# Kernel optimization log

Measured on AMD Instinct MI355X. Metric: run time of the kernel, lower is better.

## Reference

```python
import jax, jax.numpy as jnp
import numpy as np

B, S, H, DH = 2, 4096, 8, 64
D = H * DH  # 512

def setup_inputs() -> dict:
    key = jax.random.key(0)
    ks = jax.random.split(key, 9)
    sc = 1.0 / np.sqrt(D)
    return {
        "hidden_states": jax.random.normal(ks[0], (B, S, D), jnp.float32),
        "Wq": jax.random.normal(ks[1], (D, D), jnp.float32) * sc,
        "bq": jax.random.normal(ks[2], (D,), jnp.float32) * 0.02,
        "Wk": jax.random.normal(ks[3], (D, D), jnp.float32) * sc,
        "bk": jax.random.normal(ks[4], (D,), jnp.float32) * 0.02,
        "Wv": jax.random.normal(ks[5], (D, D), jnp.float32) * sc,
        "bv": jax.random.normal(ks[6], (D,), jnp.float32) * 0.02,
        "Wo": jax.random.normal(ks[7], (D, D), jnp.float32) * sc,
        "bo": jax.random.normal(ks[8], (D,), jnp.float32) * 0.02,
    }

def _split_heads(t):
    # (B, S, H*DH) -> (B, H, S, DH)
    b = t.shape[0]
    return t.reshape(b, S, H, DH).transpose(0, 2, 1, 3)

def reference(hidden_states, Wq, bq, Wk, bk, Wv, bv, Wo, bo):
    q = _split_heads(hidden_states @ Wq + bq)
    k = _split_heads(hidden_states @ Wk + bk)
    v = _split_heads(hidden_states @ Wv + bv)
    scale = 1.0 / jnp.sqrt(jnp.asarray(DH, q.dtype))
    energy = jnp.einsum('bhqd,bhkd->bhqk', q, k) * scale
    weights = jax.nn.softmax(energy, axis=-1)  # full O(S^2) matrix, as in source
    attended = jnp.einsum('bhqv,bhvd->bhqd', weights, v)
    merged = attended.transpose(0, 2, 1, 3).reshape(hidden_states.shape[0], S, D)
    return merged @ Wo + bo
```

## Files before the change

### kernel.cpp

```cpp
#include <hip/hip_runtime.h>
#include <cstdint>

typedef __bf16 bf16;
typedef __bf16 bf16x4 __attribute__((ext_vector_type(4)));
typedef __bf16 bf16x8 __attribute__((ext_vector_type(8)));
typedef float floatx4 __attribute__((ext_vector_type(4)));

#define MFMA32(a, b, c) __builtin_amdgcn_mfma_f32_16x16x32_bf16((a), (b), (c), 0, 0, 0)

__device__ inline bf16x8 cvt8(const float* p) {
    float4 u = *(const float4*)p;
    float4 v = *(const float4*)(p + 4);
    bf16x8 r;
    r[0] = (bf16)u.x; r[1] = (bf16)u.y; r[2] = (bf16)u.z; r[3] = (bf16)u.w;
    r[4] = (bf16)v.x; r[5] = (bf16)v.y; r[6] = (bf16)v.z; r[7] = (bf16)v.w;
    return r;
}

__global__ __launch_bounds__(256) void k_transpose(
    const float* __restrict__ w0, const float* __restrict__ w1,
    const float* __restrict__ w2, const float* __restrict__ w3,
    bf16* __restrict__ o0, bf16* __restrict__ o1,
    bf16* __restrict__ o2, bf16* __restrict__ o3)
{
    __shared__ float t[32][33];
    const float* in;
    bf16* out;
    switch (blockIdx.z) {
        case 0: in = w0; out = o0; break;
        case 1: in = w1; out = o1; break;
        case 2: in = w2; out = o2; break;
        default: in = w3; out = o3; break;
    }
    const int tx = threadIdx.x & 31;
    const int ty = threadIdx.x >> 5;
    const int r0 = blockIdx.y * 32;
    const int c0 = blockIdx.x * 32;
    #pragma unroll
    for (int i = 0; i < 32; i += 8)
        t[ty + i][tx] = in[(size_t)(r0 + ty + i) * 512 + c0 + tx];
    __syncthreads();
    #pragma unroll
    for (int i = 0; i < 32; i += 8)
        out[(size_t)(c0 + ty + i) * 512 + r0 + tx] = (bf16)t[tx][ty + i];
}

__global__ __launch_bounds__(256) void k_cvtx(
    const float* __restrict__ X, bf16* __restrict__ Xb)
{
    const size_t idx = ((size_t)blockIdx.x * 256 + threadIdx.x) * 8;
    *(bf16x8*)(Xb + idx) = cvt8(X + idx);
}

__global__ __launch_bounds__(256) void k_qkv(
    const bf16* __restrict__ Xb, const bf16* __restrict__ Wcat,
    const float* __restrict__ bq, const float* __restrict__ bk, const float* __restrict__ bv,
    bf16* __restrict__ Qs, bf16* __restrict__ Ks, bf16* __restrict__ Vt)
{
    __shared__ __align__(16) unsigned char smem[36864];
    uint4* Al = (uint4*)smem;
    uint4* Bl = (uint4*)(smem + 16384);

    const int tid  = threadIdx.x;
    const int w    = tid >> 6;
    const int lane = tid & 63;
    const int col  = lane & 15;
    const int quad = lane >> 4;
    const int m0 = blockIdx.x * 128;
    const int n0 = blockIdx.y * 128;

    const bf16* gA0 = Xb   + (size_t)(m0 + (tid >> 2)) * 512 + (tid & 3) * 8;
    const bf16* gA1 = gA0 + 64 * 512;
    const bf16* gB0 = Wcat + (size_t)(n0 + (tid >> 2)) * 512 + (tid & 3) * 8;
    const bf16* gB1 = gB0 + 64 * 512;

    const floatx4 zf = {0.f, 0.f, 0.f, 0.f};
    floatx4 acc[4][4];
    #pragma unroll
    for (int a = 0; a < 4; ++a)
        #pragma unroll
        for (int b = 0; b < 4; ++b) acc[a][b] = zf;

    Al[tid]       = *(const uint4*)gA0;
    Al[tid + 256] = *(const uint4*)gA1;
    Bl[tid]       = *(const uint4*)gB0;
    Bl[tid + 256] = *(const uint4*)gB1;
    __syncthreads();

    const int mb = (w & 1) * 64;
    const int nb = (w >> 1) * 64;

    int buf = 0;
    for (int kk = 0; kk < 16; ++kk) {
        const int kn = ((kk + 1) & 15) * 32;
        const uint4 pa0 = *(const uint4*)(gA0 + kn);
        const uint4 pa1 = *(const uint4*)(gA1 + kn);
        const uint4 pb0 = *(const uint4*)(gB0 + kn);
        const uint4 pb1 = *(const uint4*)(gB1 + kn);

        const uint4* A4 = Al + buf * 512;
        const uint4* B4 = Bl + buf * 512;
        bf16x8 af[4], bfr[4];
        #pragma unroll
        for (int t = 0; t < 4; ++t) {
            union { uint4 u; bf16x8 v; } ca, cb;
            ca.u = A4[(mb + 16 * t + col) * 4 + quad];
            cb.u = B4[(nb + 16 * t + col) * 4 + quad];
            af[t] = ca.v;
            bfr[t] = cb.v;
        }
        #pragma unroll
        for (int tm = 0; tm < 4; ++tm)
            #pragma unroll
            for (int tn = 0; tn < 4; ++tn)
                acc[tm][tn] = MFMA32(af[tm], bfr[tn], acc[tm][tn]);

        const int nbuf = buf ^ 1;
        Al[nbuf * 512 + tid]       = pa0;
        Al[nbuf * 512 + tid + 256] = pa1;
        Bl[nbuf * 512 + tid]       = pb0;
        Bl[nbuf * 512 + tid + 256] = pb1;
        __syncthreads();
        buf = nbuf;
    }

    bf16* ep = (bf16*)smem + (size_t)w * 64 * 72;

    const int which = blockIdx.y >> 2;
    const int nbase = (blockIdx.y & 3) * 128 + nb;
    const int h  = nbase >> 6;
    const int mw = m0 + mb;
    const int b  = mw >> 12;
    const int s0 = mw & 4095;
    const float qsc = 0.125f * 1.44269504088896f;

    if (which == 2) {
        #pragma unroll
        for (int tn = 0; tn < 4; ++tn) {
            const int d = 16 * tn + col;
            const float bb = bv[nbase + d];
            #pragma unroll
            for (int tm = 0; tm < 4; ++tm) {
                union { bf16 e[4]; uint2 u; } pk;
                #pragma unroll
                for (int r = 0; r < 4; ++r) pk.e[r] = (bf16)(acc[tm][tn][r] + bb);
                *(uint2*)(ep + d * 72 + 16 * tm + 4 * quad) = pk.u;
            }
        }
    } else {
        const float* bias = (which == 0) ? bq : bk;
        const float sc = (which == 0) ? qsc : 1.0f;
        #pragma unroll
        for (int tn = 0; tn < 4; ++tn) {
            const int d = 16 * tn + col;
            const float bb = bias[nbase + d];
            #pragma unroll
            for (int tm = 0; tm < 4; ++tm)
                #pragma unroll
                for (int r = 0; r < 4; ++r)
                    ep[(16 * tm + 4 * quad + r) * 72 + d] = (bf16)((acc[tm][tn][r] + bb) * sc);
        }
    }

    asm volatile("" ::: "memory");

    const int rl = lane >> 3;
    const int ch = lane & 7;
    bf16* gbase;
    size_t rowstride;
    if (which == 2) {
        gbase = Vt + (((size_t)b * 8 + h) * 64) * 4096 + s0;
        rowstride = 4096;
    } else {
        bf16* P = (which == 0) ? Qs : Ks;
        gbase = P + (((size_t)b * 8 + h) * 4096 + s0) * 64;
        rowstride = 64;
    }
    #pragma unroll
    for (int it = 0; it < 8; ++it) {
        const int row = it * 8 + rl;
        const uint4 v = *(const uint4*)(ep + row * 72 + ch * 8);
        *(uint4*)(gbase + (size_t)row * rowstride + ch * 8) = v;
    }
}

__global__ __launch_bounds__(512, 4) void k_attn(
    const bf16* __restrict__ Qs, const bf16* __restrict__ Ks, const bf16* __restrict__ Vt,
    bf16* __restrict__ att)
{
    __shared__ __align__(16) unsigned char smem[33280];
    uint4* Klds = (uint4*)smem;
    uint4* Vlds = (uint4*)(smem + 16384);
    float* Of   = (float*)smem;
    float* Ls   = (float*)(smem + 32768);

    const int tid  = threadIdx.x;
    const int w    = tid >> 6;
    const int hf   = w >> 2;
    const int wq   = w & 3;
    const int lane = tid & 63;
    const int col  = lane & 15;
    const int quad = lane >> 4;
    const int i    = blockIdx.x;
    const int bh   = ((i & 7) << 1) | ((i >> 3) & 1);
    const int q0   = (i >> 4) * 128 + wq * 32;

    const bf16* Qb = Qs + (size_t)bh * 262144;
    const bf16* Kb = Ks + (size_t)bh * 262144 + (size_t)hf * 2048 * 64;
    const bf16* Vb = Vt + (size_t)bh * 262144 + (size_t)hf * 2048;

    const int t8  = tid & 255;
    const int rK  = t8 >> 3;
    const int lcK = (t8 & 7) ^ (rK & 7);
    const bf16* gK = Kb + (size_t)rK * 64 + lcK * 8;
    const int pV  = t8 >> 3;
    const int ccV = (t8 & 7) ^ (pV & 7);
    const int dV  = 2 * pV + (ccV >> 2);
    const int cV  = ccV & 3;
    const bf16* gV = Vb + (size_t)dV * 4096 + cV * 8;

    uint4* Kl2 = Klds + hf * 512;
    uint4* Vl2 = Vlds + hf * 512;

    bf16x8 aq[2][2];
    #pragma unroll
    for (int s = 0; s < 2; ++s)
        #pragma unroll
        for (int c = 0; c < 2; ++c)
            aq[s][c] = *(const bf16x8*)(Qb + (size_t)(q0 + 16 * s + col) * 64 + 32 * c + quad * 8);

    const floatx4 zf = {0.f, 0.f, 0.f, 0.f};
    floatx4 o[2][4];
    float lsum[2] = {0.f, 0.f};
    #pragma unroll
    for (int s = 0; s < 2; ++s)
        #pragma unroll
        for (int dt = 0; dt < 4; ++dt) o[s][dt] = zf;

    const int c1 = col & 1, ch2 = col >> 1, qh = quad >> 1, ql = quad & 1;

    Kl2[t8] = *(const uint4*)gK;
    Vl2[t8] = *(const uint4*)gV;
    __syncthreads();

    int buf = 0;
    for (int kt = 0; kt < 2048; kt += 32) {
        const int kn = (kt + 32) & 2047;
        const uint4 kreg = *(const uint4*)(gK + (size_t)kn * 64);
        const uint4 vreg = *(const uint4*)(gV + kn);

        const uint4* Kl = Kl2 + buf * 256;
        const uint2* Vl = (const uint2*)(Vl2 + buf * 256);

        bf16x8 kf[2][2];
        #pragma unroll
        for (int t = 0; t < 2; ++t)
            #pragma unroll
            for (int c = 0; c < 2; ++c) {
                union { uint4 u; bf16x8 v; } cv;
                cv.u = Kl[(16 * t + col) * 8 + ((quad + 4 * c) ^ (col & 7))];
                kf[t][c] = cv.v;
            }
        bf16x8 vfrag8[4];
        #pragma unroll
        for (int dt = 0; dt < 4; ++dt) {
            union { uint2 u[2]; bf16x8 v; } cv;
            #pragma unroll
            for (int t = 0; t < 2; ++t) {
                const int slot = (dt * 8 + ch2) * 8 + ((c1 * 4 + 2 * t + qh) ^ ch2);
                cv.u[t] = Vl[slot * 2 + ql];
            }
            vfrag8[dt] = cv.v;
        }

        #pragma unroll
        for (int s = 0; s < 2; ++s) {
            union { bf16 e[8]; bf16x8 v; } pw;
            #pragma unroll
            for (int t = 0; t < 2; ++t) {
                floatx4 sc = MFMA32(kf[t][1], aq[s][1], MFMA32(kf[t][0], aq[s][0], zf));
                const float p0 = __builtin_amdgcn_exp2f(sc[0]);
                const float p1 = __builtin_amdgcn_exp2f(sc[1]);
                const float p2 = __builtin_amdgcn_exp2f(sc[2]);
                const float p3 = __builtin_amdgcn_exp2f(sc[3]);
                lsum[s] += (p0 + p1) + (p2 + p3);
                pw.e[4 * t + 0] = (bf16)p0; pw.e[4 * t + 1] = (bf16)p1;
                pw.e[4 * t + 2] = (bf16)p2; pw.e[4 * t + 3] = (bf16)p3;
            }
            #pragma unroll
            for (int dt = 0; dt < 4; ++dt)
                o[s][dt] = MFMA32(vfrag8[dt], pw.v, o[s][dt]);
        }

        Kl2[(buf ^ 1) * 256 + t8] = kreg;
        Vl2[(buf ^ 1) * 256 + t8] = vreg;
        __syncthreads();
        buf ^= 1;
    }

    float lv[2];
    #pragma unroll
    for (int s = 0; s < 2; ++s) {
        float v = lsum[s];
        v += __shfl_xor(v, 16, 64);
        v += __shfl_xor(v, 32, 64);
        lv[s] = v;
    }

    float* op = Of + ((size_t)(wq * 64 + lane)) * 32;
    if (hf == 1) {
        #pragma unroll
        for (int s = 0; s < 2; ++s)
            #pragma unroll
            for (int dt = 0; dt < 4; ++dt) {
                const int f = s * 4 + dt;
                *(floatx4*)(op + ((f + lane) & 7) * 4) = o[s][dt];
            }
        if (quad == 0) {
            Ls[(wq * 2 + 0) * 16 + col] = lv[0];
            Ls[(wq * 2 + 1) * 16 + col] = lv[1];
        }
    }
    __syncthreads();
    if (hf == 0) {
        float inv[2];
        #pragma unroll
        for (int s = 0; s < 2; ++s)
            inv[s] = 1.0f / (lv[s] + Ls[(wq * 2 + s) * 16 + col]);
        const int b  = bh >> 3;
        const int hh = bh & 7;
        #pragma unroll
        for (int s = 0; s < 2; ++s)
            #pragma unroll
            for (int dt = 0; dt < 4; ++dt) {
                const int f = s * 4 + dt;
                const floatx4 po = *(const floatx4*)(op + ((f + lane) & 7) * 4);
                union { bf16 e[4]; uint2 u; } pk;
                #pragma unroll
                for (int r = 0; r < 4; ++r)
                    pk.e[r] = (bf16)((o[s][dt][r] + po[r]) * inv[s]);
                const size_t row = (size_t)b * 4096 + q0 + 16 * s + col;
                *(uint2*)(att + row * 512 + hh * 64 + 16 * dt + 4 * quad) = pk.u;
            }
    }
}

__global__ __launch_bounds__(256) void k_oproj(
    const bf16* __restrict__ att, const bf16* __restrict__ Wto,
    const float* __restrict__ bo, float* __restrict__ out)
{
    __shared__ uint4 Al[2][512];
    __shared__ uint4 Bl[2][512];

    const int tid  = threadIdx.x;
    const int w    = tid >> 6;
    const int lane = tid & 63;
    const int col  = lane & 15;
    const int quad = lane >> 4;
    const int m0 = blockIdx.x * 128;
    const int n0 = blockIdx.y * 128;

    const bf16* gA0 = att + (size_t)(m0 + (tid >> 2)) * 512 + (tid & 3) * 8;
    const bf16* gA1 = gA0 + 64 * 512;
    const bf16* gB0 = Wto + (size_t)(n0 + (tid >> 2)) * 512 + (tid & 3) * 8;
    const bf16* gB1 = gB0 + 64 * 512;

    const floatx4 zf = {0.f, 0.f, 0.f, 0.f};
    floatx4 acc[4][4];
    #pragma unroll
    for (int a = 0; a < 4; ++a)
        #pragma unroll
        for (int b = 0; b < 4; ++b) acc[a][b] = zf;

    Al[0][tid]       = *(const uint4*)gA0;
    Al[0][tid + 256] = *(const uint4*)gA1;
    Bl[0][tid]       = *(const uint4*)gB0;
    Bl[0][tid + 256] = *(const uint4*)gB1;
    __syncthreads();

    const int mb = (w & 1) * 64;
    const int nb = (w >> 1) * 64;

    int buf = 0;
    for (int kk = 0; kk < 16; ++kk) {
        const int kn = ((kk + 1) & 15) * 32;
        const uint4 pa0 = *(const uint4*)(gA0 + kn);
        const uint4 pa1 = *(const uint4*)(gA1 + kn);
        const uint4 pb0 = *(const uint4*)(gB0 + kn);
        const uint4 pb1 = *(const uint4*)(gB1 + kn);

        const uint4* A4 = Al[buf];
        const uint4* B4 = Bl[buf];
        bf16x8 af[4], bfr[4];
        #pragma unroll
        for (int t = 0; t < 4; ++t) {
            union { uint4 u; bf16x8 v; } ca, cb;
            ca.u = A4[(mb + 16 * t + col) * 4 + quad];
            cb.u = B4[(nb + 16 * t + col) * 4 + quad];
            af[t] = ca.v;
            bfr[t] = cb.v;
        }
        #pragma unroll
        for (int tm = 0; tm < 4; ++tm)
            #pragma unroll
            for (int tn = 0; tn < 4; ++tn)
                acc[tm][tn] = MFMA32(af[tm], bfr[tn], acc[tm][tn]);

        Al[buf ^ 1][tid]       = pa0;
        Al[buf ^ 1][tid + 256] = pa1;
        Bl[buf ^ 1][tid]       = pb0;
        Bl[buf ^ 1][tid + 256] = pb1;
        __syncthreads();
        buf ^= 1;
    }

    #pragma unroll
    for (int tn = 0; tn < 4; ++tn) {
        const int n = n0 + nb + 16 * tn + col;
        const float bb = bo[n];
        #pragma unroll
        for (int tm = 0; tm < 4; ++tm)
            #pragma unroll
            for (int r = 0; r < 4; ++r) {
                const int m = m0 + mb + 16 * tm + quad * 4 + r;
                out[(size_t)m * 512 + n] = acc[tm][tn][r] + bb;
            }
    }
}

extern "C" void kernel_launch(void* const* d_in, const int* in_sizes, int n_in,
                              void* d_out, int out_size, void* d_ws, size_t ws_size,
                              hipStream_t stream)
{
    const float* X  = (const float*)d_in[0];
    const float* Wq = (const float*)d_in[1];
    const float* bq = (const float*)d_in[2];
    const float* Wk = (const float*)d_in[3];
    const float* bk = (const float*)d_in[4];
    const float* Wv = (const float*)d_in[5];
    const float* bv = (const float*)d_in[6];
    const float* Wo = (const float*)d_in[7];
    const float* bo = (const float*)d_in[8];

    bf16* Wtq = (bf16*)d_ws;
    bf16* Wtk = Wtq + 512 * 512;
    bf16* Wtv = Wtk + 512 * 512;
    bf16* Wto = Wtv + 512 * 512;
    bf16* Qs  = Wto + 512 * 512;
    bf16* Ks  = Qs + (size_t)16 * 4096 * 64;
    bf16* Vt  = Ks + (size_t)16 * 4096 * 64;
    bf16* att = Vt + (size_t)16 * 4096 * 64;

    bf16* Xb  = (bf16*)d_out;

    k_transpose<<<dim3(16, 16, 4), 256, 0, stream>>>(Wq, Wk, Wv, Wo, Wtq, Wtk, Wtv, Wto);
    k_cvtx<<<2048, 256, 0, stream>>>(X, Xb);
    k_qkv<<<dim3(64, 12), 256, 0, stream>>>(Xb, Wtq, bq, bk, bv, Qs, Ks, Vt);
    k_attn<<<512, 512, 0, stream>>>(Qs, Ks, Vt, att);
    k_oproj<<<dim3(64, 4), 256, 0, stream>>>(att, Wto, bo, (float*)d_out);
}
```

Before: 191.5 us.

## Merge prep kernels and stream K/V tiles into LDS via direct global loads

Fuses the weight-transpose and X-conversion kernels into one launch, which removes one kernel launch and its tail. In the attention loop, the register-staged K/V prefetch is replaced by global_load_lds, which writes global data straight into the alternate LDS buffer. This frees the VGPRs that held the prefetch and drops the explicit LDS stores. The risk is correctness, since the direct-to-LDS writes rely on the per-lane address layout matching and on the waitcnt before __syncthreads covering the async loads.

After: 201.2 us. +5.1%, slower.

```diff
diff --git a/kernel.cpp b/kernel.cpp
--- a/kernel.cpp
+++ b/kernel.cpp
@@ -7,6 +7,12 @@
 typedef float floatx4 __attribute__((ext_vector_type(4)));
 
 #define MFMA32(a, b, c) __builtin_amdgcn_mfma_f32_16x16x32_bf16((a), (b), (c), 0, 0, 0)
+
+__device__ inline void load_lds16(const void* g, void* l) {
+    __builtin_amdgcn_global_load_lds(
+        (const __attribute__((address_space(1))) void*)g,
+        (__attribute__((address_space(3))) void*)l, 16, 0, 0);
+}
 
 __device__ inline bf16x8 cvt8(const float* p) {
     float4 u = *(const float4*)p;
@@ -17,16 +23,23 @@
     return r;
 }
 
-__global__ __launch_bounds__(256) void k_transpose(
+__global__ __launch_bounds__(256) void k_prep(
+    const float* __restrict__ X, bf16* __restrict__ Xb,
     const float* __restrict__ w0, const float* __restrict__ w1,
     const float* __restrict__ w2, const float* __restrict__ w3,
     bf16* __restrict__ o0, bf16* __restrict__ o1,
     bf16* __restrict__ o2, bf16* __restrict__ o3)
 {
     __shared__ float t[32][33];
+    const int bid = blockIdx.x;
+    if (bid >= 1024) {
+        const size_t idx = ((size_t)(bid - 1024) * 256 + threadIdx.x) * 8;
+        *(bf16x8*)(Xb + idx) = cvt8(X + idx);
+        return;
+    }
     const float* in;
     bf16* out;
-    switch (blockIdx.z) {
+    switch (bid >> 8) {
         case 0: in = w0; out = o0; break;
         case 1: in = w1; out = o1; break;
         case 2: in = w2; out = o2; break;
@@ -34,8 +47,8 @@
     }
     const int tx = threadIdx.x & 31;
     const int ty = threadIdx.x >> 5;
-    const int r0 = blockIdx.y * 32;
-    const int c0 = blockIdx.x * 32;
+    const int r0 = ((bid >> 4) & 15) * 32;
+    const int c0 = (bid & 15) * 32;
     #pragma unroll
     for (int i = 0; i < 32; i += 8)
         t[ty + i][tx] = in[(size_t)(r0 + ty + i) * 512 + c0 + tx];
@@ -43,13 +56,6 @@
     #pragma unroll
     for (int i = 0; i < 32; i += 8)
         out[(size_t)(c0 + ty + i) * 512 + r0 + tx] = (bf16)t[tx][ty + i];
-}
-
-__global__ __launch_bounds__(256) void k_cvtx(
-    const float* __restrict__ X, bf16* __restrict__ Xb)
-{
-    const size_t idx = ((size_t)blockIdx.x * 256 + threadIdx.x) * 8;
-    *(bf16x8*)(Xb + idx) = cvt8(X + idx);
 }
 
 __global__ __launch_bounds__(256) void k_qkv(
@@ -239,15 +245,15 @@
 
     const int c1 = col & 1, ch2 = col >> 1, qh = quad >> 1, ql = quad & 1;
 
-    Kl2[t8] = *(const uint4*)gK;
-    Vl2[t8] = *(const uint4*)gV;
+    load_lds16(gK, &Kl2[t8]);
+    load_lds16(gV, &Vl2[t8]);
     __syncthreads();
 
     int buf = 0;
     for (int kt = 0; kt < 2048; kt += 32) {
         const int kn = (kt + 32) & 2047;
-        const uint4 kreg = *(const uint4*)(gK + (size_t)kn * 64);
-        const uint4 vreg = *(const uint4*)(gV + kn);
+        load_lds16(gK + (size_t)kn * 64, &Kl2[(buf ^ 1) * 256 + t8]);
+        load_lds16(gV + kn,              &Vl2[(buf ^ 1) * 256 + t8]);
 
         const uint4* Kl = Kl2 + buf * 256;
         const uint2* Vl = (const uint2*)(Vl2 + buf * 256);
@@ -292,8 +298,6 @@
                 o[s][dt] = MFMA32(vfrag8[dt], pw.v, o[s][dt]);
         }
 
-        Kl2[(buf ^ 1) * 256 + t8] = kreg;
-        Vl2[(buf ^ 1) * 256 + t8] = vreg;
         __syncthreads();
         buf ^= 1;
     }
@@ -453,8 +457,7 @@
 
     bf16* Xb  = (bf16*)d_out;
 
-    k_transpose<<<dim3(16, 16, 4), 256, 0, stream>>>(Wq, Wk, Wv, Wo, Wtq, Wtk, Wtv, Wto);
-    k_cvtx<<<2048, 256, 0, stream>>>(X, Xb);
+    k_prep<<<3072, 256, 0, stream>>>(X, Xb, Wq, Wk, Wv, Wo, Wtq, Wtk, Wtv, Wto);
     k_qkv<<<dim3(64, 12), 256, 0, stream>>>(Xb, Wtq, bq, bk, bv, Qs, Ks, Vt);
     k_attn<<<512, 512, 0, stream>>>(Qs, Ks, Vt, att);
     k_oproj<<<dim3(64, 4), 256, 0, stream>>>(att, Wto, bo, (float*)d_out);
```
